# Kernel optimization log

Measured on AMD Instinct MI355X. Metric: run time of the kernel, lower is better.

Reference implementation:

```python
import jax, jax.numpy as jnp
import numpy as np

B, S, M, D, H, DH = 2, 1024, 1024, 1024, 16, 64
K = S + M                 # key length
R = 2 * K - 1             # relative position table width
EPS = 1e-5


def layer_norm(x, gamma, beta):
    mu = jnp.mean(x, axis=-1, keepdims=True)
    var = jnp.mean(jnp.square(x - mu), axis=-1, keepdims=True)
    return (x - mu) * jax.lax.rsqrt(var + EPS) * gamma + beta


def skew(q_pos, mem_len):
    # q_pos: (B, H, L, R) with R = 2*k_len - 1
    b, h, L, r = q_pos.shape
    pad = jnp.full((b, h, L, 1), -jnp.inf, q_pos.dtype)
    x = jnp.concatenate([q_pos, pad], axis=-1).reshape(b, h, L * (r + 1))
    x = x[..., : L * r].reshape(b, h, L, r)
    k_len = (r + 1) // 2
    start = k_len - 1 - mem_len
    return x[..., start : start + k_len]  # (B, H, L, k_len)


def setup_inputs() -> dict:
    key = jax.random.key(0)
    ks = jax.random.split(key, 9)
    hidden = jax.random.normal(ks[0], (B, S, D), jnp.float32)
    memory = jax.random.normal(ks[1], (B, M, D), jnp.float32)
    pos_emb = jax.random.normal(ks[2], (B, R, DH), jnp.float32)
    # causal mask: query i may attend keys j <= i + M ; True = blocked
    mask = jnp.arange(K)[None, :] > (jnp.arange(S)[:, None] + M)
    sc = 1.0 / np.sqrt(D)
    Wq = jax.random.normal(ks[3], (D, H * DH), jnp.float32) * sc
    Wk = jax.random.normal(ks[4], (D, H * DH), jnp.float32) * sc
    Wv = jax.random.normal(ks[5], (D, H * DH), jnp.float32) * sc
    Wo = jax.random.normal(ks[6], (H * DH, D), jnp.float32) * sc
    gamma = jnp.ones((D,), jnp.float32)
    beta = jnp.zeros((D,), jnp.float32)
    return {"hidden": hidden, "pos_emb": pos_emb, "memory": memory,
            "mask": mask, "Wq": Wq, "Wk": Wk, "Wv": Wv, "Wo": Wo,
            "gamma": gamma, "beta": beta}


def reference(hidden, pos_emb, memory, mask, Wq, Wk, Wv, Wo, gamma, beta):
    mem_len = memory.shape[1]
    combined = jnp.concatenate([memory, hidden], axis=1)  # (B, K, D)
    h_ln = layer_norm(hidden, gamma, beta)                # pre-LN
    c_ln = layer_norm(combined, gamma, beta)
    q = (h_ln @ Wq).reshape(B, S, H, DH).transpose(0, 2, 1, 3)  # (B,H,S,DH)
    k = (c_ln @ Wk).reshape(B, K, H, DH).transpose(0, 2, 1, 3)  # (B,H,K,DH)
    v = (c_ln @ Wv).reshape(B, K, H, DH).transpose(0, 2, 1, 3)
    score = jnp.einsum('bhsd,bhkd->bhsk', q, k)                  # (B,H,S,K)
    q_pos = jnp.einsum('bhsd,brd->bhsr', q, pos_emb)             # (B,H,S,R)
    score = (score + skew(q_pos, mem_len)) * (1.0 / np.sqrt(D))
    score = jnp.where(mask[None, None], -jnp.inf, score)
    p = jax.nn.softmax(score, axis=-1)
    attn = jnp.einsum('bhsk,bhkd->bshd', p, v).reshape(B, S, H * DH)
    out = attn @ Wo
    return h_ln + out
```

## Files before the change

### kernel.cpp

```cpp
#include <hip/hip_runtime.h>
#include <hip/hip_bf16.h>

#define B_ 2
#define S_ 1024
#define M_ 1024
#define D_ 1024
#define H_ 16
#define DH_ 64
#define K_ 2048
#define R_ 4095

#define NEG_BIG (-1e30f)

typedef unsigned short u16;
typedef short short8 __attribute__((ext_vector_type(8)));
typedef float f32x4 __attribute__((ext_vector_type(4)));

__device__ __forceinline__ u16 f2bf(float f) {
  __hip_bfloat16 h = __float2bfloat16(f);
  return *reinterpret_cast<u16*>(&h);
}
__device__ __forceinline__ float bf2f(u16 u) {
  __hip_bfloat16 h;
  *reinterpret_cast<u16*>(&h) = u;
  return __bfloat162float(h);
}

__device__ __forceinline__ void gll16(const void* g, const void* l) {
  __builtin_amdgcn_global_load_lds(
      (const __attribute__((address_space(1))) unsigned int*)g,
      (__attribute__((address_space(3))) unsigned int*)l, 16, 0, 0);
}

__device__ __forceinline__ f32x4 mfma16(short8 a, short8 b, f32x4 c) {
  return __builtin_amdgcn_mfma_f32_16x16x32_bf16(a, b, c, 0, 0, 0);
}

__global__ __launch_bounds__(256) void prep_kernel(
    const float* __restrict__ hidden, const float* __restrict__ memory,
    const float* __restrict__ gamma, const float* __restrict__ beta,
    u16* __restrict__ cln,
    const float* __restrict__ W0, const float* __restrict__ W1,
    const float* __restrict__ W2, const float* __restrict__ W3,
    u16* __restrict__ O0, u16* __restrict__ O1,
    u16* __restrict__ O2, u16* __restrict__ O3,
    const float* __restrict__ pos, u16* __restrict__ posT) {
  __shared__ u16 tile[64][66];
  __shared__ float red[8];
  const int bx = blockIdx.x;
  const int t = threadIdx.x;

  if (bx < 4096) {
    const int b = bx >> 11;
    const int idx = bx & (K_ - 1);
    const float* src = (idx < M_)
        ? memory + (size_t)(b * M_ + idx) * D_
        : hidden + (size_t)(b * S_ + (idx - M_)) * D_;
    const int lane = t & 63, w = t >> 6;
    float4 rv = ((const float4*)src)[t];
    float s = rv.x + rv.y + rv.z + rv.w;
    float ss = rv.x * rv.x + rv.y * rv.y + rv.z * rv.z + rv.w * rv.w;
#pragma unroll
    for (int m = 1; m < 64; m <<= 1) {
      s += __shfl_xor(s, m, 64);
      ss += __shfl_xor(ss, m, 64);
    }
    if (lane == 0) { red[w] = s; red[4 + w] = ss; }
    __syncthreads();
    s = red[0] + red[1] + red[2] + red[3];
    ss = red[4] + red[5] + red[6] + red[7];
    const float mu = s * (1.0f / D_);
    const float var = ss * (1.0f / D_) - mu * mu;
    const float rstd = rsqrtf(var + 1e-5f);
    float4 gv = ((const float4*)gamma)[t];
    float4 bv = ((const float4*)beta)[t];
    ushort4 ov;
    ov.x = f2bf((rv.x - mu) * rstd * gv.x + bv.x);
    ov.y = f2bf((rv.y - mu) * rstd * gv.y + bv.y);
    ov.z = f2bf((rv.z - mu) * rstd * gv.z + bv.z);
    ov.w = f2bf((rv.w - mu) * rstd * gv.w + bv.w);
    ((ushort4*)(cln + (size_t)bx * D_))[t] = ov;
    return;
  }
  if (bx < 5120) {
    const int z = (bx - 4096) >> 8;
    const int rem = (bx - 4096) & 255;
    const float* in; u16* out;
    switch (z) {
      case 0:  in = W0; out = O0; break;
      case 1:  in = W1; out = O1; break;
      case 2:  in = W2; out = O2; break;
      default: in = W3; out = O3; break;
    }
    const int tx = t & 63, ty = t >> 6;
    const int k0 = (rem & 15) * 64, n0 = (rem >> 4) * 64;
#pragma unroll
    for (int i = ty; i < 64; i += 4)
      tile[i][tx] = f2bf(in[(size_t)(k0 + i) * D_ + n0 + tx]);
    __syncthreads();
#pragma unroll
    for (int i = ty; i < 64; i += 4)
      out[(size_t)(n0 + i) * D_ + k0 + tx] = tile[tx][i];
    return;
  }
  {
    const int u = (bx - 5120) * 256 + t;
    const int oct = u & 7;
    const int r = (u >> 3) & 15;
    const int g = (u >> 7) % 136;
    const int b = u / 17408;
    const int row = g * 16 + r;
    const float* s = pos + ((size_t)b * R_ + row) * 64 + oct * 8;
    float4 v0 = ((const float4*)s)[0];
    float4 v1 = ((const float4*)s)[1];
    ushort4 oA, oB;
    oA.x = f2bf(v0.x); oA.y = f2bf(v0.y); oA.z = f2bf(v0.z); oA.w = f2bf(v0.w);
    oB.x = f2bf(v1.x); oB.y = f2bf(v1.y); oB.z = f2bf(v1.z); oB.w = f2bf(v1.w);
    u16* d = posT + (size_t)(b * 144 + g) * 1024 + oct * 128 + r * 8;
    ((ushort4*)d)[0] = oA;
    ((ushort4*)d)[1] = oB;
  }
}

__device__ __forceinline__ int maprow_hidden(int r) {
  return r + ((r >> 10) << 10) + M_;
}

__global__ __launch_bounds__(256, 3) void gemm_qkv_kernel(
    const u16* __restrict__ A, const u16* __restrict__ Bt,
    u16* __restrict__ qb, u16* __restrict__ kb, u16* __restrict__ vbT) {
  __shared__ __align__(16) u16 shm[128 * 132];
  u16* As = shm;
  u16* Bs = shm + 8192;
  const int t = threadIdx.x;
  const int lane = t & 63, w = t >> 6;
  const int wm = w >> 1, wn = w & 1;
  const int qd = lane >> 4, lr = lane & 15;
  const int m0 = blockIdx.y * 128, n0 = blockIdx.x * 128;
  if (n0 < 1024 && !(m0 & 1024)) return;

  const int swz = ((t & 7) ^ ((t >> 3) & 7)) * 8;
  const int c0 = (qd ^ (lr & 7)) * 8;
  const int c1 = c0 ^ 32;
  const int row8 = (t >> 3) & 7;

  f32x4 acc[4][4];
#pragma unroll
  for (int mt = 0; mt < 4; mt++)
#pragma unroll
    for (int nt = 0; nt < 4; nt++) acc[mt][nt] = (f32x4){0.f, 0.f, 0.f, 0.f};

  for (int kt = 0; kt < 1024; kt += 64) {
#pragma unroll
    for (int p = 0; p < 4; p++) {
      const int ra = w * 32 + p * 8 + row8;
      gll16(A + (size_t)(m0 + ra) * 1024 + kt + swz, As + (w * 32 + p * 8) * 64);
      gll16(Bt + (size_t)(n0 + ra) * 1024 + kt + swz, Bs + (w * 32 + p * 8) * 64);
    }
    __syncthreads();
    short8 a0[4], a1[4], b0[4], b1[4];
#pragma unroll
    for (int mt = 0; mt < 4; mt++) {
      a0[mt] = *(const short8*)&As[(wm * 64 + mt * 16 + lr) * 64 + c0];
      a1[mt] = *(const short8*)&As[(wm * 64 + mt * 16 + lr) * 64 + c1];
    }
#pragma unroll
    for (int nt = 0; nt < 4; nt++) {
      b0[nt] = *(const short8*)&Bs[(wn * 64 + nt * 16 + lr) * 64 + c0];
      b1[nt] = *(const short8*)&Bs[(wn * 64 + nt * 16 + lr) * 64 + c1];
    }
#pragma unroll
    for (int mt = 0; mt < 4; mt++)
#pragma unroll
      for (int nt = 0; nt < 4; nt++) {
        acc[mt][nt] = mfma16(a0[mt], b0[nt], acc[mt][nt]);
        acc[mt][nt] = mfma16(a1[mt], b1[nt], acc[mt][nt]);
      }
    __syncthreads();
  }

  const bool isV = (n0 >= 2048);
  if (!isV) {
    const float sc = (n0 < 1024) ? 0.03125f : 1.0f;
#pragma unroll
    for (int mt = 0; mt < 4; mt++)
#pragma unroll
      for (int nt = 0; nt < 4; nt++) {
        const int row0 = wm * 64 + mt * 16 + qd * 4;
        const int col = wn * 64 + nt * 16 + lr;
#pragma unroll
        for (int r = 0; r < 4; r++)
          shm[(row0 + r) * 132 + col] = f2bf(acc[mt][nt][r] * sc);
      }
  } else {
#pragma unroll
    for (int mt = 0; mt < 4; mt++)
#pragma unroll
      for (int nt = 0; nt < 4; nt++) {
        const int kk0 = wm * 64 + mt * 16 + qd * 4;
        const int nn = wn * 64 + nt * 16 + lr;
        ushort4 pk;
        pk.x = f2bf(acc[mt][nt][0]);
        pk.y = f2bf(acc[mt][nt][1]);
        pk.z = f2bf(acc[mt][nt][2]);
        pk.w = f2bf(acc[mt][nt][3]);
        *(ushort4*)&shm[nn * 132 + kk0] = pk;
      }
  }
  __syncthreads();
  const int bq = m0 >> 11;
#pragma unroll
  for (int i = 0; i < 8; i++) {
    const int flat = i * 256 + t;
    const int row = flat >> 4;
    const int ch = flat & 15;
    const ushort4 v0 = *(const ushort4*)&shm[row * 132 + ch * 8];
    const ushort4 v1 = *(const ushort4*)&shm[row * 132 + ch * 8 + 4];
    u16* dst;
    if (n0 < 1024) {
      const int qrow = (bq << 10) | ((m0 + row) & 1023);
      dst = qb + (size_t)qrow * 1024 + n0 + ch * 8;
    } else if (!isV) {
      const int key = (m0 + row) & (K_ - 1);
      dst = kb + (size_t)(bq * K_ + key) * 1024 + (n0 - 1024) + ch * 8;
    } else {
      const int dhg = (n0 - 2048) + row;
      const int bh = (bq << 4) | (dhg >> 6);
      const int dh = dhg & 63;
      dst = vbT + (size_t)(bh * 64 + dh) * K_ + (m0 & (K_ - 1)) + ch * 8;
    }
    short8 vv;
    *(ushort4*)&vv = v0;
    *(((ushort4*)&vv) + 1) = v1;
    *(short8*)dst = vv;
  }
}

__global__ __launch_bounds__(256, 2) void out_gemm_kernel(
    const u16* __restrict__ A, const u16* __restrict__ Bt,
    const u16* __restrict__ resid, float* __restrict__ Cf) {
  __shared__ __align__(16) u16 As[128 * 64];
  __shared__ __align__(16) u16 Bs[64 * 64];
  const int t = threadIdx.x;
  const int lane = t & 63, w = t >> 6;
  const int wm = w >> 1, wn = w & 1;
  const int qd = lane >> 4, lr = lane & 15;
  const int m0 = blockIdx.y * 128, n0 = blockIdx.x * 64;

  const int swz = ((t & 7) ^ ((t >> 3) & 7)) * 8;
  const int c0 = (qd ^ (lr & 7)) * 8;
  const int c1 = c0 ^ 32;
  const int row8 = (t >> 3) & 7;

  f32x4 acc[4][2];
#pragma unroll
  for (int mt = 0; mt < 4; mt++)
#pragma unroll
    for (int nt = 0; nt < 2; nt++) acc[mt][nt] = (f32x4){0.f, 0.f, 0.f, 0.f};

  for (int kt = 0; kt < 1024; kt += 64) {
#pragma unroll
    for (int p = 0; p < 4; p++) {
      const int ra = w * 32 + p * 8 + row8;
      gll16(A + (size_t)(m0 + ra) * 1024 + kt + swz, As + (w * 32 + p * 8) * 64);
    }
#pragma unroll
    for (int p = 0; p < 2; p++) {
      const int rb = w * 16 + p * 8 + row8;
      gll16(Bt + (size_t)(n0 + rb) * 1024 + kt + swz, Bs + (w * 16 + p * 8) * 64);
    }
    __syncthreads();
    short8 a0[4], a1[4], b0[2], b1[2];
#pragma unroll
    for (int mt = 0; mt < 4; mt++) {
      a0[mt] = *(const short8*)&As[(wm * 64 + mt * 16 + lr) * 64 + c0];
      a1[mt] = *(const short8*)&As[(wm * 64 + mt * 16 + lr) * 64 + c1];
    }
#pragma unroll
    for (int nt = 0; nt < 2; nt++) {
      b0[nt] = *(const short8*)&Bs[(wn * 32 + nt * 16 + lr) * 64 + c0];
      b1[nt] = *(const short8*)&Bs[(wn * 32 + nt * 16 + lr) * 64 + c1];
    }
#pragma unroll
    for (int mt = 0; mt < 4; mt++)
#pragma unroll
      for (int nt = 0; nt < 2; nt++) {
        acc[mt][nt] = mfma16(a0[mt], b0[nt], acc[mt][nt]);
        acc[mt][nt] = mfma16(a1[mt], b1[nt], acc[mt][nt]);
      }
    __syncthreads();
  }

#pragma unroll
  for (int mt = 0; mt < 4; mt++)
#pragma unroll
    for (int nt = 0; nt < 2; nt++)
#pragma unroll
      for (int r = 0; r < 4; r++) {
        const int row = m0 + wm * 64 + mt * 16 + qd * 4 + r;
        const int col = n0 + wn * 32 + nt * 16 + lr;
        float v = acc[mt][nt][r] + bf2f(resid[(size_t)maprow_hidden(row) * 1024 + col]);
        Cf[(size_t)row * 1024 + col] = v;
      }
}

__global__ __launch_bounds__(256, 2) void attn_kernel(
    const u16* __restrict__ qb, const u16* __restrict__ kb,
    const u16* __restrict__ vbT, const u16* __restrict__ posT,
    u16* __restrict__ ab) {
  __shared__ __align__(16) u16 Ks[2][2][64 * 64];
  __shared__ __align__(16) u16 Vt[2][2][64 * 64];
  __shared__ __align__(16) u16 Pt[4][16 * 64];

  const int t = threadIdx.x;
  const int lane = t & 63, w = t >> 6;
  const int qd = lane >> 4, lr = lane & 15;

  const int flat = blockIdx.x + 16 * blockIdx.y + 256 * blockIdx.z;
  const int xcd = flat & 7;
  const int slot = flat >> 3;
  const int gsub = slot >> 4;
  int qt = slot & 15;
  if (gsub & 2) qt = 15 - qt;
  const int g = gsub * 8 + xcd;
  const int h = g & 15;
  const int b = g >> 4;
  const int i0 = qt * 64;

  const int swz = ((t & 7) ^ ((t >> 3) & 7)) * 8;
  const int c0 = (qd ^ (lr & 7)) * 8;
  const int c1 = c0 ^ 32;
  const int row8 = t >> 3;

  const int jmax = min(K_, i0 + 64 + M_);

  const int g0 = 63 - (i0 >> 4) - w;
  const u16* pb0 = posT + (size_t)b * 147456 + qd * 128 + lr * 8;

#pragma unroll
  for (int rd = 0; rd < 2; rd++)
    gll16(qb + (size_t)(b * S_ + i0 + rd * 32 + row8) * 1024 + h * 64 + swz,
          &Ks[1][0][0] + rd * 2048 + w * 512);
#pragma unroll
  for (int sb = 0; sb < 2; sb++)
#pragma unroll
    for (int rd = 0; rd < 2; rd++) {
      gll16(kb + (size_t)(b * K_ + sb * 64 + rd * 32 + row8) * 1024 + h * 64 + swz,
            &Ks[0][sb][0] + rd * 2048 + w * 512);
      gll16(vbT + (size_t)((b * H_ + h) * 64 + rd * 32 + row8) * K_ + sb * 64 + swz,
            &Vt[0][sb][0] + rd * 2048 + w * 512);
    }
  short8 pgA0[5], pgA1[5], pgB0[5], pgB1[5];
  {
    const u16* pp = pb0 + (size_t)g0 * 1024;
#pragma unroll
    for (int pc = 0; pc < 5; pc++) {
      pgA0[pc] = *(const short8*)(pp + pc * 1024);
      pgA1[pc] = *(const short8*)(pp + pc * 1024 + 512);
    }
    const u16* p2 = pb0 + (size_t)(g0 + 4) * 1024;
#pragma unroll
    for (int pc = 0; pc < 5; pc++) {
      pgB0[pc] = *(const short8*)(p2 + pc * 1024);
      pgB1[pc] = *(const short8*)(p2 + pc * 1024 + 512);
    }
  }
  __syncthreads();
  const short8 aQ0 = *(const short8*)&Ks[1][0][(w * 16 + lr) * 64 + c0];
  const short8 aQ1 = *(const short8*)&Ks[1][0][(w * 16 + lr) * 64 + c1];

  f32x4 accO[4];
#pragma unroll
  for (int d = 0; d < 4; d++) accO[d] = (f32x4){0.f, 0.f, 0.f, 0.f};
  float lsum[4];
#pragma unroll
  for (int r = 0; r < 4; r++) lsum[r] = 0.f;

  for (int j0 = 0, ph = 0; j0 < jmax; j0 += 128, ph++) {
    __syncthreads();
    const int cb = ph & 1;
    const int nb = cb ^ 1;
    const int j0n = j0 + 128;
#pragma unroll
    for (int sb = 0; sb < 2; sb++)
      if (j0n + sb * 64 < jmax) {
#pragma unroll
        for (int rd = 0; rd < 2; rd++) {
          gll16(kb + (size_t)(b * K_ + j0n + sb * 64 + rd * 32 + row8) * 1024 + h * 64 + swz,
                &Ks[nb][sb][0] + rd * 2048 + w * 512);
          gll16(vbT + (size_t)((b * H_ + h) * 64 + rd * 32 + row8) * K_ + j0n + sb * 64 + swz,
                &Vt[nb][sb][0] + rd * 2048 + w * 512);
        }
      }

    {
      __builtin_amdgcn_s_setprio(1);
      f32x4 zp[5];
#pragma unroll
      for (int pc = 0; pc < 5; pc++) {
        f32x4 z = {0.f, 0.f, 0.f, 0.f};
        z = mfma16(aQ0, pgA0[pc], z);
        zp[pc] = mfma16(aQ1, pgA1[pc], z);
      }
      f32x4 sqk[4];
#pragma unroll
      for (int kc = 0; kc < 4; kc++) {
        const short8 bK0 = *(const short8*)&Ks[cb][0][(kc * 16 + lr) * 64 + c0];
        const short8 bK1 = *(const short8*)&Ks[cb][0][(kc * 16 + lr) * 64 + c1];
        f32x4 z = {0.f, 0.f, 0.f, 0.f};
        z = mfma16(aQ0, bK0, z);
        sqk[kc] = mfma16(aQ1, bK1, z);
      }
      __builtin_amdgcn_s_setprio(0);
      {
        const u16* pn = pb0 + (size_t)(g0 + 4 * (2 * ph + 2)) * 1024;
#pragma unroll
        for (int pc = 0; pc < 5; pc++) {
          pgA0[pc] = *(const short8*)(pn + pc * 1024);
          pgA1[pc] = *(const short8*)(pn + pc * 1024 + 512);
        }
      }
      const bool tail = (j0 + 63 > i0 + w * 16 + M_);
      float p[4][4];
#pragma unroll
      for (int r = 0; r < 4; r++) {
        const int iL = qd * 4 + r;
        const int d = 15 + lr - iL;
        const int srcl = qd * 16 + (d & 15);
        const bool hi = (d >> 4) & 1;
        float g0s = __shfl(zp[0][r], srcl, 64);
        float g1s = __shfl(zp[1][r], srcl, 64);
        float g2s = __shfl(zp[2][r], srcl, 64);
        float g3s = __shfl(zp[3][r], srcl, 64);
        float g4s = __shfl(zp[4][r], srcl, 64);
        float s0 = sqk[0][r] + (hi ? g1s : g0s);
        float s1 = sqk[1][r] + (hi ? g2s : g1s);
        float s2 = sqk[2][r] + (hi ? g3s : g2s);
        float s3 = sqk[3][r] + (hi ? g4s : g3s);
        if (tail) {
          const int key = j0 + lr, lim = i0 + w * 16 + iL + M_;
          if (key      > lim) s0 = NEG_BIG;
          if (key + 16 > lim) s1 = NEG_BIG;
          if (key + 32 > lim) s2 = NEG_BIG;
          if (key + 48 > lim) s3 = NEG_BIG;
        }
        p[0][r] = __expf(s0);
        p[1][r] = __expf(s1);
        p[2][r] = __expf(s2);
        p[3][r] = __expf(s3);
        lsum[r] += p[0][r] + p[1][r] + p[2][r] + p[3][r];
      }
#pragma unroll
      for (int r = 0; r < 4; r++) {
        const int row = qd * 4 + r;
        const int cbase = row * 64;
        const int rx = row & 7;
        const int lo = lr & 7, hi8 = lr >> 3;
#pragma unroll
        for (int kc = 0; kc < 4; kc++)
          Pt[w][cbase + ((((kc << 1) | hi8) ^ rx) << 3) + lo] = f2bf(p[kc][r]);
      }
      __asm__ volatile("s_waitcnt lgkmcnt(0)" ::: "memory");
      const short8 aP0 = *(const short8*)&Pt[w][lr * 64 + ((qd ^ (lr & 7)) << 3)];
      const short8 aP1 = *(const short8*)&Pt[w][lr * 64 + (((qd + 4) ^ (lr & 7)) << 3)];
      __builtin_amdgcn_s_setprio(1);
#pragma unroll
      for (int d2 = 0; d2 < 4; d2++) {
        const short8 bV0 = *(const short8*)&Vt[cb][0][(d2 * 16 + lr) * 64 + c0];
        const short8 bV1 = *(const short8*)&Vt[cb][0][(d2 * 16 + lr) * 64 + c1];
        accO[d2] = mfma16(aP0, bV0, accO[d2]);
        accO[d2] = mfma16(aP1, bV1, accO[d2]);
      }
      __builtin_amdgcn_s_setprio(0);
    }

    if (j0 + 64 < jmax) {
      const int j1 = j0 + 64;
      __builtin_amdgcn_s_setprio(1);
      f32x4 zp[5];
#pragma unroll
      for (int pc = 0; pc < 5; pc++) {
        f32x4 z = {0.f, 0.f, 0.f, 0.f};
        z = mfma16(aQ0, pgB0[pc], z);
        zp[pc] = mfma16(aQ1, pgB1[pc], z);
      }
      f32x4 sqk[4];
#pragma unroll
      for (int kc = 0; kc < 4; kc++) {
        const short8 bK0 = *(const short8*)&Ks[cb][1][(kc * 16 + lr) * 64 + c0];
        const short8 bK1 = *(const short8*)&Ks[cb][1][(kc * 16 + lr) * 64 + c1];
        f32x4 z = {0.f, 0.f, 0.f, 0.f};
        z = mfma16(aQ0, bK0, z);
        sqk[kc] = mfma16(aQ1, bK1, z);
      }
      __builtin_amdgcn_s_setprio(0);
      {
        const u16* pn = pb0 + (size_t)(g0 + 4 * (2 * ph + 3)) * 1024;
#pragma unroll
        for (int pc = 0; pc < 5; pc++) {
          pgB0[pc] = *(const short8*)(pn + pc * 1024);
          pgB1[pc] = *(const short8*)(pn + pc * 1024 + 512);
        }
      }
      const bool tail = (j1 + 63 > i0 + w * 16 + M_);
      float p[4][4];
#pragma unroll
      for (int r = 0; r < 4; r++) {
        const int iL = qd * 4 + r;
        const int d = 15 + lr - iL;
        const int srcl = qd * 16 + (d & 15);
        const bool hi = (d >> 4) & 1;
        float g0s = __shfl(zp[0][r], srcl, 64);
        float g1s = __shfl(zp[1][r], srcl, 64);
        float g2s = __shfl(zp[2][r], srcl, 64);
        float g3s = __shfl(zp[3][r], srcl, 64);
        float g4s = __shfl(zp[4][r], srcl, 64);
        float s0 = sqk[0][r] + (hi ? g1s : g0s);
        float s1 = sqk[1][r] + (hi ? g2s : g1s);
        float s2 = sqk[2][r] + (hi ? g3s : g2s);
        float s3 = sqk[3][r] + (hi ? g4s : g3s);
        if (tail) {
          const int key = j1 + lr, lim = i0 + w * 16 + iL + M_;
          if (key      > lim) s0 = NEG_BIG;
          if (key + 16 > lim) s1 = NEG_BIG;
          if (key + 32 > lim) s2 = NEG_BIG;
          if (key + 48 > lim) s3 = NEG_BIG;
        }
        p[0][r] = __expf(s0);
        p[1][r] = __expf(s1);
        p[2][r] = __expf(s2);
        p[3][r] = __expf(s3);
        lsum[r] += p[0][r] + p[1][r] + p[2][r] + p[3][r];
      }
#pragma unroll
      for (int r = 0; r < 4; r++) {
        const int row = qd * 4 + r;
        const int cbase = row * 64;
        const int rx = row & 7;
        const int lo = lr & 7, hi8 = lr >> 3;
#pragma unroll
        for (int kc = 0; kc < 4; kc++)
          Pt[w][cbase + ((((kc << 1) | hi8) ^ rx) << 3) + lo] = f2bf(p[kc][r]);
      }
      __asm__ volatile("s_waitcnt lgkmcnt(0)" ::: "memory");
      const short8 aP0 = *(const short8*)&Pt[w][lr * 64 + ((qd ^ (lr & 7)) << 3)];
      const short8 aP1 = *(const short8*)&Pt[w][lr * 64 + (((qd + 4) ^ (lr & 7)) << 3)];
      __builtin_amdgcn_s_setprio(1);
#pragma unroll
      for (int d2 = 0; d2 < 4; d2++) {
        const short8 bV0 = *(const short8*)&Vt[cb][1][(d2 * 16 + lr) * 64 + c0];
        const short8 bV1 = *(const short8*)&Vt[cb][1][(d2 * 16 + lr) * 64 + c1];
        accO[d2] = mfma16(aP0, bV0, accO[d2]);
        accO[d2] = mfma16(aP1, bV1, accO[d2]);
      }
      __builtin_amdgcn_s_setprio(0);
    }
  }

  float inv[4];
#pragma unroll
  for (int r = 0; r < 4; r++) {
#pragma unroll
    for (int msk = 1; msk < 16; msk <<= 1) lsum[r] += __shfl_xor(lsum[r], msk, 64);
    inv[r] = 1.0f / lsum[r];
  }
#pragma unroll
  for (int d2 = 0; d2 < 4; d2++)
#pragma unroll
    for (int r = 0; r < 4; r++) {
      const int iG = i0 + w * 16 + qd * 4 + r;
      ab[(size_t)(b * S_ + iG) * 1024 + h * 64 + d2 * 16 + lr] = f2bf(accO[d2][r] * inv[r]);
    }
}

extern "C" void kernel_launch(void* const* d_in, const int* in_sizes, int n_in,
                              void* d_out, int out_size, void* d_ws, size_t ws_size,
                              hipStream_t stream) {
  const float* hidden = (const float*)d_in[0];
  const float* pos    = (const float*)d_in[1];
  const float* memory = (const float*)d_in[2];
  const float* Wq = (const float*)d_in[4];
  const float* Wk = (const float*)d_in[5];
  const float* Wv = (const float*)d_in[6];
  const float* Wo = (const float*)d_in[7];
  const float* gamma = (const float*)d_in[8];
  const float* beta  = (const float*)d_in[9];

  char* ws = (char*)d_ws;
  u16* cln  = (u16*)(ws);
  u16* qb   = (u16*)(ws + 8388608);
  u16* kb   = (u16*)(ws + 12582912);
  u16* vbT  = (u16*)(ws + 20971520);
  u16* ab   = (u16*)(ws + 29360128);
  u16* WqT  = (u16*)(ws + 33554432);
  u16* WkT  = WqT + 1048576;
  u16* WvT  = WkT + 1048576;
  u16* WoT  = WvT + 1048576;
  u16* posT = (u16*)(ws + 41943040);

  prep_kernel<<<dim3(5256), 256, 0, stream>>>(
      hidden, memory, gamma, beta, cln,
      Wq, Wk, Wv, Wo, WqT, WkT, WvT, WoT, pos, posT);
  gemm_qkv_kernel<<<dim3(24, 32), 256, 0, stream>>>(cln, WqT, qb, kb, vbT);
  attn_kernel<<<dim3(S_ / 64, H_, B_), 256, 0, stream>>>(qb, kb, vbT, posT, ab);
  out_gemm_kernel<<<dim3(16, 16), 256, 0, stream>>>(ab, WoT, cln, (float*)d_out);
}
```

Measured before the change: 193.6 us.

## Store V in MFMA fragment layout and load directly to registers in attention

The QKV GEMM epilogue now writes V into a per-64-key-tile layout that matches the MFMA B-operand fragment order. The attention kernel then loads V straight from global memory into registers, so the V shared-memory buffers and their async copies go away. The weight-transpose prep step also switches to float4 loads and ushort4 stores. The aim is to free LDS and cut LDS traffic, at the cost of global-load latency landing inside the loop with no explicit prefetch.

```diff
diff --git a/kernel.cpp b/kernel.cpp
--- a/kernel.cpp
+++ b/kernel.cpp
@@ -92,15 +92,28 @@
       case 2:  in = W2; out = O2; break;
       default: in = W3; out = O3; break;
     }
-    const int tx = t & 63, ty = t >> 6;
     const int k0 = (rem & 15) * 64, n0 = (rem >> 4) * 64;
-#pragma unroll
-    for (int i = ty; i < 64; i += 4)
-      tile[i][tx] = f2bf(in[(size_t)(k0 + i) * D_ + n0 + tx]);
+    const int c4 = t & 15, rr = t >> 4;
+#pragma unroll
+    for (int p = 0; p < 4; p++) {
+      const int i = rr + p * 16;
+      float4 v = *(const float4*)&in[(size_t)(k0 + i) * D_ + n0 + c4 * 4];
+      tile[i][c4 * 4 + 0] = f2bf(v.x);
+      tile[i][c4 * 4 + 1] = f2bf(v.y);
+      tile[i][c4 * 4 + 2] = f2bf(v.z);
+      tile[i][c4 * 4 + 3] = f2bf(v.w);
+    }
     __syncthreads();
 #pragma unroll
-    for (int i = ty; i < 64; i += 4)
-      out[(size_t)(n0 + i) * D_ + k0 + tx] = tile[tx][i];
+    for (int p = 0; p < 4; p++) {
+      const int i = rr + p * 16;
+      ushort4 o;
+      o.x = tile[c4 * 4 + 0][i];
+      o.y = tile[c4 * 4 + 1][i];
+      o.z = tile[c4 * 4 + 2][i];
+      o.w = tile[c4 * 4 + 3][i];
+      *(ushort4*)&out[(size_t)(n0 + i) * D_ + k0 + c4 * 4] = o;
+    }
     return;
   }
   {
@@ -128,7 +141,7 @@
 
 __global__ __launch_bounds__(256, 3) void gemm_qkv_kernel(
     const u16* __restrict__ A, const u16* __restrict__ Bt,
-    u16* __restrict__ qb, u16* __restrict__ kb, u16* __restrict__ vbT) {
+    u16* __restrict__ qb, u16* __restrict__ kb, u16* __restrict__ vf) {
   __shared__ __align__(16) u16 shm[128 * 132];
   u16* As = shm;
   u16* Bs = shm + 8192;
@@ -227,7 +240,12 @@
       const int dhg = (n0 - 2048) + row;
       const int bh = (bq << 4) | (dhg >> 6);
       const int dh = dhg & 63;
-      dst = vbT + (size_t)(bh * 64 + dh) * K_ + (m0 & (K_ - 1)) + ch * 8;
+      const int gk = (m0 & (K_ - 1)) + ch * 8;
+      const int ktile = gk >> 6;
+      const int w6ch = (gk & 63) >> 3;
+      const int d2 = dh >> 4, lrr = dh & 15;
+      dst = vf + (size_t)bh * 131072 + (size_t)ktile * 4096
+               + ((d2 * 8 + w6ch) * 16 + lrr) * 8;
     }
     short8 vv;
     *(ushort4*)&vv = v0;
@@ -306,10 +324,9 @@
 
 __global__ __launch_bounds__(256, 2) void attn_kernel(
     const u16* __restrict__ qb, const u16* __restrict__ kb,
-    const u16* __restrict__ vbT, const u16* __restrict__ posT,
+    const u16* __restrict__ vf, const u16* __restrict__ posT,
     u16* __restrict__ ab) {
   __shared__ __align__(16) u16 Ks[2][2][64 * 64];
-  __shared__ __align__(16) u16 Vt[2][2][64 * 64];
   __shared__ __align__(16) u16 Pt[4][16 * 64];
 
   const int t = threadIdx.x;
@@ -336,6 +353,7 @@
 
   const int g0 = 63 - (i0 >> 4) - w;
   const u16* pb0 = posT + (size_t)b * 147456 + qd * 128 + lr * 8;
+  const u16* vfb = vf + (size_t)(b * H_ + h) * 131072 + lr * 8;
 
 #pragma unroll
   for (int rd = 0; rd < 2; rd++)
@@ -344,12 +362,9 @@
 #pragma unroll
   for (int sb = 0; sb < 2; sb++)
 #pragma unroll
-    for (int rd = 0; rd < 2; rd++) {
+    for (int rd = 0; rd < 2; rd++)
       gll16(kb + (size_t)(b * K_ + sb * 64 + rd * 32 + row8) * 1024 + h * 64 + swz,
             &Ks[0][sb][0] + rd * 2048 + w * 512);
-      gll16(vbT + (size_t)((b * H_ + h) * 64 + rd * 32 + row8) * K_ + sb * 64 + swz,
-            &Vt[0][sb][0] + rd * 2048 + w * 512);
-    }
   short8 pgA0[5], pgA1[5], pgB0[5], pgB1[5];
   {
     const u16* pp = pb0 + (size_t)g0 * 1024;
@@ -385,15 +400,19 @@
     for (int sb = 0; sb < 2; sb++)
       if (j0n + sb * 64 < jmax) {
 #pragma unroll
-        for (int rd = 0; rd < 2; rd++) {
+        for (int rd = 0; rd < 2; rd++)
           gll16(kb + (size_t)(b * K_ + j0n + sb * 64 + rd * 32 + row8) * 1024 + h * 64 + swz,
                 &Ks[nb][sb][0] + rd * 2048 + w * 512);
-          gll16(vbT + (size_t)((b * H_ + h) * 64 + rd * 32 + row8) * K_ + j0n + sb * 64 + swz,
-                &Vt[nb][sb][0] + rd * 2048 + w * 512);
-        }
       }
 
     {
+      const u16* vtp = vfb + (size_t)(j0 >> 6) * 4096;
+      short8 vA[4], vB[4];
+#pragma unroll
+      for (int d2 = 0; d2 < 4; d2++) {
+        vA[d2] = *(const short8*)(vtp + (d2 * 8 + qd) * 128);
+        vB[d2] = *(const short8*)(vtp + (d2 * 8 + qd + 4) * 128);
+      }
       __builtin_amdgcn_s_setprio(1);
       f32x4 zp[5];
 #pragma unroll
@@ -466,16 +485,21 @@
       __builtin_amdgcn_s_setprio(1);
 #pragma unroll
       for (int d2 = 0; d2 < 4; d2++) {
-        const short8 bV0 = *(const short8*)&Vt[cb][0][(d2 * 16 + lr) * 64 + c0];
-        const short8 bV1 = *(const short8*)&Vt[cb][0][(d2 * 16 + lr) * 64 + c1];
-        accO[d2] = mfma16(aP0, bV0, accO[d2]);
-        accO[d2] = mfma16(aP1, bV1, accO[d2]);
+        accO[d2] = mfma16(aP0, vA[d2], accO[d2]);
+        accO[d2] = mfma16(aP1, vB[d2], accO[d2]);
       }
       __builtin_amdgcn_s_setprio(0);
     }
 
     if (j0 + 64 < jmax) {
       const int j1 = j0 + 64;
+      const u16* vtp = vfb + (size_t)(j1 >> 6) * 4096;
+      short8 vA[4], vB[4];
+#pragma unroll
+      for (int d2 = 0; d2 < 4; d2++) {
+        vA[d2] = *(const short8*)(vtp + (d2 * 8 + qd) * 128);
+        vB[d2] = *(const short8*)(vtp + (d2 * 8 + qd + 4) * 128);
+      }
       __builtin_amdgcn_s_setprio(1);
       f32x4 zp[5];
 #pragma unroll
@@ -548,10 +572,8 @@
       __builtin_amdgcn_s_setprio(1);
 #pragma unroll
       for (int d2 = 0; d2 < 4; d2++) {
-        const short8 bV0 = *(const short8*)&Vt[cb][1][(d2 * 16 + lr) * 64 + c0];
-        const short8 bV1 = *(const short8*)&Vt[cb][1][(d2 * 16 + lr) * 64 + c1];
-        accO[d2] = mfma16(aP0, bV0, accO[d2]);
-        accO[d2] = mfma16(aP1, bV1, accO[d2]);
+        accO[d2] = mfma16(aP0, vA[d2], accO[d2]);
+        accO[d2] = mfma16(aP1, vB[d2], accO[d2]);
       }
       __builtin_amdgcn_s_setprio(0);
     }
@@ -590,7 +612,7 @@
   u16* cln  = (u16*)(ws);
   u16* qb   = (u16*)(ws + 8388608);
   u16* kb   = (u16*)(ws + 12582912);
-  u16* vbT  = (u16*)(ws + 20971520);
+  u16* vf   = (u16*)(ws + 20971520);
   u16* ab   = (u16*)(ws + 29360128);
   u16* WqT  = (u16*)(ws + 33554432);
   u16* WkT  = WqT + 1048576;
@@ -601,7 +623,7 @@
   prep_kernel<<<dim3(5256), 256, 0, stream>>>(
       hidden, memory, gamma, beta, cln,
       Wq, Wk, Wv, Wo, WqT, WkT, WvT, WoT, pos, posT);
-  gemm_qkv_kernel<<<dim3(24, 32), 256, 0, stream>>>(cln, WqT, qb, kb, vbT);
-  attn_kernel<<<dim3(S_ / 64, H_, B_), 256, 0, stream>>>(qb, kb, vbT, posT, ab);
+  gemm_qkv_kernel<<<dim3(24, 32), 256, 0, stream>>>(cln, WqT, qb, kb, vf);
+  attn_kernel<<<dim3(S_ / 64, H_, B_), 256, 0, stream>>>(qb, kb, vf, posT, ab);
   out_gemm_kernel<<<dim3(16, 16), 256, 0, stream>>>(ab, WoT, cln, (float*)d_out);
 }
```

After: 193.8 us. No clear change (+0.1%).
